# Optimization experiments

Hardware: AMD Instinct MI355X
Metric: run time of the kernel (lower is better)

The kernel has to match this reference:

```python
import jax, jax.numpy as jnp
import numpy as np

NPOINT = 1024
RADIUS = 0.2
NSAMPLE = 32
BN_EPS = 1e-5


def setup_inputs() -> dict:
    key = jax.random.key(0)
    ks = jax.random.split(key, 8)
    B, N, D = 16, 8192, 9
    xyz = jax.random.uniform(ks[0], (B, N, 3), dtype=jnp.float32)
    points = jax.random.normal(ks[1], (B, N, D), dtype=jnp.float32)
    chans = [D, 64, 64, 128]
    inp = {"xyz": xyz, "points": points}
    for i in range(3):
        cin, cout = chans[i], chans[i + 1]
        inp[f"W{i}"] = jax.random.normal(ks[2 + i], (cout, cin), dtype=jnp.float32) / np.sqrt(cin).astype(np.float32)
        inp[f"b{i}"] = jnp.zeros((cout,), jnp.float32)
        inp[f"gamma{i}"] = jnp.ones((cout,), jnp.float32)
        inp[f"beta{i}"] = jnp.zeros((cout,), jnp.float32)
    return inp


def farthest_point_sample(xyz, npoint):
    # xyz: [B,N,3]. Sequential FPS via lax.scan (deterministic start at index 0).
    B, N, _ = xyz.shape
    dist0 = jnp.full((B, N), 1e10, xyz.dtype)
    far0 = jnp.zeros((B,), jnp.int32)

    def step(carry, _):
        distance, farthest = carry
        centroid = jnp.take_along_axis(xyz, farthest[:, None, None], axis=1)  # [B,1,3]
        d = jnp.sum((xyz - centroid) ** 2, axis=-1)  # [B,N]
        distance = jnp.minimum(distance, d)
        return (distance, jnp.argmax(distance, axis=-1).astype(jnp.int32)), farthest

    (_, _), cents = jax.lax.scan(step, (dist0, far0), None, length=npoint)
    return cents.T  # [B,npoint]


def gather_points(points, idx):
    # points [B,N,C], idx [B,...] -> [B,...,C]
    return jax.vmap(lambda p, i: p[i])(points, idx)


def query_ball_point(radius, nsample, xyz, new_xyz):
    # pairwise squared distances [B,S,N]
    sqr = (jnp.sum(new_xyz ** 2, -1)[:, :, None]
           + jnp.sum(xyz ** 2, -1)[:, None, :]
           - 2.0 * jnp.einsum('bsc,bnc->bsn', new_xyz, xyz))
    negd, idx = jax.lax.top_k(-sqr, nsample)  # nsample nearest, ascending distance
    d = -negd
    first = idx[:, :, :1]
    return jnp.where(d > radius ** 2, first, idx)  # [B,S,nsample]


def reference(xyz, points, W0, b0, gamma0, beta0, W1, b1, gamma1, beta1, W2, b2, gamma2, beta2):
    cent = farthest_point_sample(xyz, NPOINT)          # [B,S]
    new_xyz = gather_points(xyz, cent)                  # [B,S,3]
    idx = query_ball_point(RADIUS, NSAMPLE, xyz, new_xyz)
    x = gather_points(points, idx)                      # [B,S,K,D]
    x = jnp.transpose(x, (0, 3, 2, 1))                  # [B,D,K,S]
    for W, b, g, be in ((W0, b0, gamma0, beta0), (W1, b1, gamma1, beta1), (W2, b2, gamma2, beta2)):
        x = jnp.einsum('oc,bcks->boks', W, x) + b[None, :, None, None]
        mean = x.mean(axis=(0, 2, 3), keepdims=True)    # training-mode BatchNorm2d
        var = x.var(axis=(0, 2, 3), keepdims=True)
        x = (x - mean) * jax.lax.rsqrt(var + BN_EPS) * g[None, :, None, None] + be[None, :, None, None]
        x = jax.nn.relu(x)
    feat = jnp.max(x, axis=2)                           # max over nsample -> [B,C,S]
    return new_xyz, jnp.transpose(feat, (0, 2, 1))      # [B,S,3], [B,S,128]
```

## Files before the change

### kernel.cpp

```cpp
#include <hip/hip_runtime.h>
#include <cstddef>
#include <cstdint>


#define BB 16
#define NN 8192
#define DD 9
#define SS 1024
#define KK 32
#define M_COLS (BB*SS*KK)
#define C1 64
#define C2 64
#define C3 128
#define NBKT 64
#define NG 54

#define WSB_IDX   0
#define WSB_STATS (WSB_IDX + M_COLS*2)
#define WSB_AFF   (WSB_STATS + 32768*4)
#define WSB_WT    (WSB_AFF + 512*4)
#define WSB_END   (WSB_WT + 12864*4)
#define WSB_Y2    ((WSB_END + 255) & ~255)
#define PG1 0
#define PS2 (2*NBKT*C1)
#define PQ2 (3*NBKT*C1)
#define PS3 (4*NBKT*C1)
#define PQ3 (PS3 + NBKT*C3)

__device__ __forceinline__ unsigned wave_umax_dpp(unsigned v) {
    int x = (int)v, t;
    t = __builtin_amdgcn_update_dpp(x, x, 0x111, 0xf, 0xf, false);
    x = ((unsigned)t > (unsigned)x) ? t : x;
    t = __builtin_amdgcn_update_dpp(x, x, 0x112, 0xf, 0xf, false);
    x = ((unsigned)t > (unsigned)x) ? t : x;
    t = __builtin_amdgcn_update_dpp(x, x, 0x114, 0xf, 0xf, false);
    x = ((unsigned)t > (unsigned)x) ? t : x;
    t = __builtin_amdgcn_update_dpp(x, x, 0x118, 0xf, 0xf, false);
    x = ((unsigned)t > (unsigned)x) ? t : x;
    t = __builtin_amdgcn_update_dpp(x, x, 0x142, 0xf, 0xf, false);
    x = ((unsigned)t > (unsigned)x) ? t : x;
    t = __builtin_amdgcn_update_dpp(x, x, 0x143, 0xf, 0xf, false);
    x = ((unsigned)t > (unsigned)x) ? t : x;
    return (unsigned)__builtin_amdgcn_readlane(x, 63);
}

#define FPS_T   512
#define FPS_PPT (NN/FPS_T)
#define FPS_W   (FPS_T/64)

__global__ __launch_bounds__(FPS_T) void fps_kernel(const float* __restrict__ xyz,
                                                    float* __restrict__ out_newxyz) {
    __shared__ float sx[NN], sy[NN], sz[NN];
    __shared__ int   sfar[SS];
    __shared__ unsigned long long rp[2][FPS_W];
    const int b = blockIdx.x, tid = threadIdx.x;
    const int wave = tid >> 6, lane = tid & 63;
    const float* base = xyz + (size_t)b * NN * 3;
    for (int i = tid; i < NN; i += FPS_T) {
        sx[i] = base[i*3+0];
        sy[i] = base[i*3+1];
        sz[i] = base[i*3+2];
    }
    __syncthreads();
    float px[FPS_PPT], py[FPS_PPT], pz[FPS_PPT], dist[FPS_PPT];
#pragma unroll
    for (int m = 0; m < FPS_PPT; ++m) {
        int i = tid + m*FPS_T;
        px[m] = sx[i]; py[m] = sy[i]; pz[m] = sz[i];
        dist[m] = 1e10f;
    }
    if (tid == 0) sfar[0] = 0;
    float cx = sx[0], cy = sy[0], cz = sz[0];
    for (int it = 1; it < SS; ++it) {
        float lv = -1.0f; int lm = 0;
#pragma unroll
        for (int m = 0; m < FPS_PPT; ++m) {
            float dx = px[m]-cx, dy = py[m]-cy, dz = pz[m]-cz;
            float d  = fmaf(dz, dz, fmaf(dy, dy, dx*dx));
            float nd = fminf(dist[m], d);
            dist[m] = nd;
            if (nd > lv) { lv = nd; lm = m; }
        }
        int li = tid + lm*FPS_T;
        unsigned uv  = __float_as_uint(lv);
        unsigned wvu = wave_umax_dpp(uv);
        unsigned ci  = (uv == wvu) ? (unsigned)(NN - 1 - li) : 0u;
        unsigned cm  = wave_umax_dpp(ci);
        const int pb = it & 1;
        if (lane == 0) rp[pb][wave] = ((unsigned long long)wvu << 32) | cm;
        __syncthreads();
        unsigned long long bp = rp[pb][0];
#pragma unroll
        for (int w = 1; w < FPS_W; ++w) {
            unsigned long long o = rp[pb][w];
            bp = (o > bp) ? o : bp;
        }
        int bi = NN - 1 - (int)(unsigned int)(bp & 0xFFFFFFFFull);
        if (tid == 0) sfar[it] = bi;
        cx = sx[bi]; cy = sy[bi]; cz = sz[bi];
    }
    __syncthreads();
    for (int s = tid; s < SS; s += FPS_T) {
        int nidx = sfar[s];
        out_newxyz[((size_t)b*SS + s)*3 + 0] = sx[nidx];
        out_newxyz[((size_t)b*SS + s)*3 + 1] = sy[nidx];
        out_newxyz[((size_t)b*SS + s)*3 + 2] = sz[nidx];
    }
}

__device__ __forceinline__ unsigned fmap(float f) {
    unsigned u = __float_as_uint(f);
    return u ^ (unsigned)(((int)u >> 31) | 0x80000000);
}
#define PK_INF 0xFFFFFFFFFFFFFFFFull

__global__ __launch_bounds__(64) void query_kernel(const float* __restrict__ xyz,
                                                   const float* __restrict__ newxyz,
                                                   unsigned short* __restrict__ idx_out) {
    __shared__ unsigned bm[NN/32];
    const int blk  = blockIdx.x;
    const int b    = blk >> 10;
    const int lane = threadIdx.x;
    for (int i = lane; i < NN/32; i += 64) bm[i] = 0;
    const float cx = newxyz[(size_t)blk*3+0];
    const float cy = newxyz[(size_t)blk*3+1];
    const float cz = newxyz[(size_t)blk*3+2];
    const float s2 = fmaf(cz, cz, fmaf(cy, cy, cx*cx));
    const float* xb = xyz + (size_t)b*NN*3;
    float lv = 3.0e38f; int li = 0;
    for (int m = 0; m < NN/64; ++m) {
        int j = lane + m*64;
        float x = xb[(size_t)j*3+0], y = xb[(size_t)j*3+1], z = xb[(size_t)j*3+2];
        float n2  = fmaf(z, z, fmaf(y, y, x*x));
        float dot = fmaf(cz, z, fmaf(cy, y, cx*x));
        float sq  = (s2 + n2) - 2.0f*dot;
        if (sq < lv) { lv = sq; li = j; }
    }
    __syncthreads();
    unsigned long long lpk = ((unsigned long long)fmap(lv) << 32) | (unsigned)li;
    unsigned long long g = lpk;
#pragma unroll
    for (int msk = 1; msk < 64; msk <<= 1) {
        unsigned long long o = __shfl_xor(g, msk, 64);
        g = (o < g) ? o : g;
    }
    const unsigned R2M = fmap(0.04f);
    int first_idx = 0, out_idx = 0;
    for (int k = 0; k < KK; ++k) {
        int wi = (int)(unsigned)(g & 0xFFFFFFFFull);
        unsigned wm = (unsigned)(g >> 32);
        if (k == 0) first_idx = wi;
        int keep = (wm > R2M) ? first_idx : wi;
        if (lane == k) out_idx = keep;
        int owner = wi & 63;
        if (lane == owner) bm[wi >> 5] |= (1u << (wi & 31));
        __syncthreads();
        int j0 = owner + ((2*lane) << 6);
        int j1 = j0 + 64;
        float x0 = xb[(size_t)j0*3+0], y0 = xb[(size_t)j0*3+1], z0 = xb[(size_t)j0*3+2];
        float x1 = xb[(size_t)j1*3+0], y1 = xb[(size_t)j1*3+1], z1 = xb[(size_t)j1*3+2];
        float sq0 = (s2 + fmaf(z0, z0, fmaf(y0, y0, x0*x0))) - 2.0f*fmaf(cz, z0, fmaf(cy, y0, cx*x0));
        float sq1 = (s2 + fmaf(z1, z1, fmaf(y1, y1, x1*x1))) - 2.0f*fmaf(cz, z1, fmaf(cy, y1, cx*x1));
        bool t0 = (bm[j0 >> 5] >> (j0 & 31)) & 1;
        bool t1 = (bm[j1 >> 5] >> (j1 & 31)) & 1;
        unsigned long long p0 = t0 ? PK_INF : (((unsigned long long)fmap(sq0) << 32) | (unsigned)j0);
        unsigned long long p1 = t1 ? PK_INF : (((unsigned long long)fmap(sq1) << 32) | (unsigned)j1);
        unsigned long long r = (p1 < p0) ? p1 : p0;
        unsigned long long c = (lane == owner) ? PK_INF : lpk;
        c = (r < c) ? r : c;
#pragma unroll
        for (int msk = 1; msk < 64; msk <<= 1) {
            unsigned long long ro = __shfl_xor(r, msk, 64);
            unsigned long long co = __shfl_xor(c, msk, 64);
            r = (ro < r) ? ro : r;
            c = (co < c) ? co : c;
        }
        if (lane == owner) lpk = r;
        g = c;
        __syncthreads();
    }
    if (lane < KK) idx_out[(size_t)blk*KK + lane] = (unsigned short)out_idx;
}

__global__ void transpose_w_kernel(const float* __restrict__ W0, const float* __restrict__ W1,
                                   const float* __restrict__ W2, float* __restrict__ w0t,
                                   float* __restrict__ w1t, float* __restrict__ w2t) {
    int t = blockIdx.x*256 + threadIdx.x;
    if (t < DD*C1)  { int c = t / C1, o = t % C1; w0t[t] = W0[o*DD + c]; }
    if (t < C1*C2)  { int c = t / C2, o = t % C2; w1t[t] = W1[o*C1 + c]; }
    if (t < C1*C3)  { int c = t / C3, o = t % C3; w2t[t] = W2[o*C1 + c]; }
}

__global__ __launch_bounds__(256) void gram_kernel(const float* __restrict__ points,
                                                   const unsigned short* __restrict__ idxw,
                                                   float* __restrict__ pg) {
    __shared__ float sg[NG];
    const int tid = threadIdx.x, lane = tid & 63;
    float acc[NG];
#pragma unroll
    for (int t = 0; t < NG; ++t) acc[t] = 0.f;
#pragma unroll
    for (int i = 0; i < 4; ++i) {
        int col = blockIdx.x*1024 + i*256 + tid;
        int n = idxw[col];
        int b = col >> 15;
        const float* p = points + ((size_t)b*NN + n)*DD;
        float x[DD];
#pragma unroll
        for (int c = 0; c < DD; ++c) x[c] = p[c];
#pragma unroll
        for (int c = 0; c < DD; ++c) acc[c] += x[c];
        int t = DD;
#pragma unroll
        for (int c = 0; c < DD; ++c)
#pragma unroll
            for (int d = c; d < DD; ++d) { acc[t] = fmaf(x[c], x[d], acc[t]); ++t; }
    }
#pragma unroll
    for (int t = 0; t < NG; ++t) {
#pragma unroll
        for (int msk = 1; msk < 64; msk <<= 1) acc[t] += __shfl_xor(acc[t], msk, 64);
    }
    if (tid < NG) sg[tid] = 0.f;
    __syncthreads();
    if (lane == 0) {
#pragma unroll
        for (int t = 0; t < NG; ++t) atomicAdd(&sg[t], acc[t]);
    }
    __syncthreads();
    int bkt = blockIdx.x & (NBKT-1);
    if (tid < NG) atomicAdd(&pg[bkt*64 + tid], sg[tid]);
}

__global__ void affine1_kernel(const float* __restrict__ pg,
                               const float* __restrict__ W0, const float* __restrict__ b0,
                               const float* __restrict__ gamma, const float* __restrict__ beta,
                               float* __restrict__ scale, float* __restrict__ shift) {
    __shared__ float sm[NG];
    int tid = threadIdx.x;
    if (tid < NG) {
        float s = 0.f;
        for (int b = 0; b < NBKT; ++b) s += pg[b*64 + tid];
        sm[tid] = s;
    }
    __syncthreads();
    if (tid < C1) {
        float w[DD];
#pragma unroll
        for (int i = 0; i < DD; ++i) w[i] = W0[tid*DD + i];
        float mv = 0.f;
#pragma unroll
        for (int i = 0; i < DD; ++i) mv = fmaf(w[i], sm[i], mv);
        float q = 0.f;
        int t = DD;
#pragma unroll
        for (int c = 0; c < DD; ++c)
#pragma unroll
            for (int d = c; d < DD; ++d) {
                float coef = w[c]*w[d];
                if (c != d) coef = coef + coef;
                q = fmaf(coef, sm[t], q); ++t;
            }
        float b0v = b0[tid];
        const float M = (float)M_COLS;
        float s_sum = mv + M*b0v;
        float s_sq  = q + 2.f*b0v*mv + M*b0v*b0v;
        const float invM = 1.0f / M;
        float mean = s_sum * invM;
        float var  = s_sq * invM - mean*mean;
        float sc   = gamma[tid] / sqrtf(var + 1e-5f);
        scale[tid] = sc;
        shift[tid] = beta[tid] - mean*sc;
    }
}

__device__ __forceinline__ void stats_accumulate64(const float* acc,
                                                   float* __restrict__ g_sum,
                                                   float* __restrict__ g_sq) {
    __shared__ float s_sum[C1];
    __shared__ float s_sq[C1];
    int tid = threadIdx.x, lane = tid & 63;
    if (tid < C1) { s_sum[tid] = 0.f; s_sq[tid] = 0.f; }
    __syncthreads();
#pragma unroll
    for (int o = 0; o < C1; ++o) {
        float v = acc[o];
        float q = v*v;
#pragma unroll
        for (int msk = 1; msk < 64; msk <<= 1) {
            v += __shfl_xor(v, msk, 64);
            q += __shfl_xor(q, msk, 64);
        }
        if (lane == 0) { atomicAdd(&s_sum[o], v); atomicAdd(&s_sq[o], q); }
    }
    __syncthreads();
    if (tid < C1) { atomicAdd(&g_sum[tid], s_sum[tid]); atomicAdd(&g_sq[tid], s_sq[tid]); }
    __syncthreads();
}

__device__ __forceinline__ void gather_conv1(const float* __restrict__ points,
                                             const unsigned short* __restrict__ idxw,
                                             const float* __restrict__ w0t,
                                             const float* __restrict__ b0,
                                             int col, float (&a1)[C1]) {
    int n = idxw[col];
    int b = col >> 15;
    const float* p = points + ((size_t)b*NN + n)*DD;
    float x[DD];
#pragma unroll
    for (int c = 0; c < DD; ++c) x[c] = p[c];
#pragma unroll
    for (int o = 0; o < C1; ++o) a1[o] = b0[o];
#pragma unroll
    for (int c = 0; c < DD; ++c) {
        float xc = x[c];
#pragma unroll
        for (int o = 0; o < C1; ++o) a1[o] = fmaf(w0t[c*C1+o], xc, a1[o]);
    }
}

__device__ __forceinline__ void conv2_from_a1(float (&a1)[C1],
                                              const float* __restrict__ sc1,
                                              const float* __restrict__ sh1,
                                              const float* __restrict__ w1t,
                                              const float* __restrict__ b1,
                                              float (&a2)[C2]) {
#pragma unroll
    for (int c = 0; c < C1; ++c) a1[c] = fmaxf(fmaf(a1[c], sc1[c], sh1[c]), 0.0f);
#pragma unroll
    for (int o = 0; o < C2; ++o) a2[o] = b1[o];
    for (int c = 0; c < C1; ++c) {
        float xc = a1[c];
#pragma unroll
        for (int o = 0; o < C2; ++o) a2[o] = fmaf(w1t[c*C2+o], xc, a2[o]);
    }
}

__global__ void affine_kernel(const float* __restrict__ psum, const float* __restrict__ psq,
                              const float* __restrict__ gamma, const float* __restrict__ beta,
                              float* __restrict__ scale, float* __restrict__ shift, int nch) {
    int i = threadIdx.x;
    if (i < nch) {
        float s = 0.f, q = 0.f;
        for (int b = 0; b < NBKT; ++b) { s += psum[b*nch + i]; q += psq[b*nch + i]; }
        const float invM = 1.0f / (float)M_COLS;
        float mean = s * invM;
        float var  = q * invM - mean*mean;
        float sc   = gamma[i] / sqrtf(var + 1e-5f);
        scale[i] = sc;
        shift[i] = beta[i] - mean*sc;
    }
}

template<bool STORE>
__device__ __forceinline__ void pass2_body(const float* __restrict__ points,
                                           const unsigned short* __restrict__ idxw,
                                           const float* __restrict__ w0t,
                                           const float* __restrict__ b0,
                                           const float* __restrict__ sc1,
                                           const float* __restrict__ sh1,
                                           const float* __restrict__ w1t,
                                           const float* __restrict__ b1,
                                           float* __restrict__ Y2,
                                           float* __restrict__ pstats) {
    int col = blockIdx.x*256 + threadIdx.x;
    int bkt = blockIdx.x & (NBKT-1);
    float a1[C1], a2[C2];
    gather_conv1(points, idxw, w0t, b0, col, a1);
    conv2_from_a1(a1, sc1, sh1, w1t, b1, a2);
    if (STORE) {
#pragma unroll
        for (int o = 0; o < C2; ++o) Y2[(size_t)o*M_COLS + col] = a2[o];
    }
    stats_accumulate64(a2, pstats + PS2 + bkt*C1, pstats + PQ2 + bkt*C1);
}

__global__ __launch_bounds__(256) void pass2_kernel(const float* __restrict__ points,
                                                    const unsigned short* __restrict__ idxw,
                                                    const float* __restrict__ w0t,
                                                    const float* __restrict__ b0,
                                                    const float* __restrict__ sc1,
                                                    const float* __restrict__ sh1,
                                                    const float* __restrict__ w1t,
                                                    const float* __restrict__ b1,
                                                    float* __restrict__ pstats) {
    pass2_body<false>(points, idxw, w0t, b0, sc1, sh1, w1t, b1, nullptr, pstats);
}

__global__ __launch_bounds__(256) void pass2_store_kernel(const float* __restrict__ points,
                                                          const unsigned short* __restrict__ idxw,
                                                          const float* __restrict__ w0t,
                                                          const float* __restrict__ b0,
                                                          const float* __restrict__ sc1,
                                                          const float* __restrict__ sh1,
                                                          const float* __restrict__ w1t,
                                                          const float* __restrict__ b1,
                                                          float* __restrict__ Y2,
                                                          float* __restrict__ pstats) {
    pass2_body<true>(points, idxw, w0t, b0, sc1, sh1, w1t, b1, Y2, pstats);
}

__device__ __forceinline__ void pass34_tail(float (&a2)[C2],
                                            const float* __restrict__ sc2,
                                            const float* __restrict__ sh2,
                                            const float* __restrict__ w2t,
                                            const float* __restrict__ b2,
                                            const float* __restrict__ gamma2,
                                            float* __restrict__ pool_out,
                                            float* __restrict__ pstats) {
#pragma unroll
    for (int c = 0; c < C2; ++c) a2[c] = fmaxf(fmaf(a2[c], sc2[c], sh2[c]), 0.0f);
    int col = blockIdx.x*256 + threadIdx.x;
    int bkt = blockIdx.x & (NBKT-1);
    int lane = threadIdx.x & 63;
    int bs = col >> 5;
#pragma unroll
    for (int h = 0; h < 2; ++h) {
        float acc[C1];
#pragma unroll
        for (int o = 0; o < C1; ++o) acc[o] = b2[h*C1+o];
        for (int c = 0; c < C2; ++c) {
            float xc = a2[c];
#pragma unroll
            for (int o = 0; o < C1; ++o) acc[o] = fmaf(w2t[c*C3 + h*C1 + o], xc, acc[o]);
        }
#pragma unroll
        for (int o = 0; o < C1; ++o) {
            bool pos = gamma2[h*C1+o] >= 0.f;
            float v = pos ? acc[o] : -acc[o];
#pragma unroll
            for (int msk = 1; msk < 32; msk <<= 1) v = fmaxf(v, __shfl_xor(v, msk, 64));
            if ((lane & 31) == 0) pool_out[(size_t)bs*C3 + h*C1 + o] = pos ? v : -v;
        }
        stats_accumulate64(acc, pstats + PS3 + bkt*C3 + h*C1, pstats + PQ3 + bkt*C3 + h*C1);
    }
}

__global__ __launch_bounds__(256) void pass34_kernel(const float* __restrict__ points,
                                                     const unsigned short* __restrict__ idxw,
                                                     const float* __restrict__ w0t,
                                                     const float* __restrict__ b0,
                                                     const float* __restrict__ sc1,
                                                     const float* __restrict__ sh1,
                                                     const float* __restrict__ w1t,
                                                     const float* __restrict__ b1,
                                                     const float* __restrict__ sc2,
                                                     const float* __restrict__ sh2,
                                                     const float* __restrict__ w2t,
                                                     const float* __restrict__ b2,
                                                     const float* __restrict__ gamma2,
                                                     float* __restrict__ pool_out,
                                                     float* __restrict__ pstats) {
    int col = blockIdx.x*256 + threadIdx.x;
    float a1[C1], a2[C2];
    gather_conv1(points, idxw, w0t, b0, col, a1);
    conv2_from_a1(a1, sc1, sh1, w1t, b1, a2);
    pass34_tail(a2, sc2, sh2, w2t, b2, gamma2, pool_out, pstats);
}

__global__ __launch_bounds__(256) void pass34_cached_kernel(const float* __restrict__ Y2,
                                                            const float* __restrict__ sc2,
                                                            const float* __restrict__ sh2,
                                                            const float* __restrict__ w2t,
                                                            const float* __restrict__ b2,
                                                            const float* __restrict__ gamma2,
                                                            float* __restrict__ pool_out,
                                                            float* __restrict__ pstats) {
    int col = blockIdx.x*256 + threadIdx.x;
    float a2[C2];
#pragma unroll
    for (int o = 0; o < C2; ++o) a2[o] = Y2[(size_t)o*M_COLS + col];
    pass34_tail(a2, sc2, sh2, w2t, b2, gamma2, pool_out, pstats);
}

__global__ __launch_bounds__(256) void bn3relu_kernel(float* __restrict__ pool,
                                                      const float* __restrict__ sc3,
                                                      const float* __restrict__ sh3) {
    int e = blockIdx.x*256 + threadIdx.x;
    int ch = e & (C3-1);
    float v = pool[e];
    pool[e] = fmaxf(fmaf(v, sc3[ch], sh3[ch]), 0.0f);
}

extern "C" void kernel_launch(void* const* d_in, const int* in_sizes, int n_in,
                              void* d_out, int out_size, void* d_ws, size_t ws_size,
                              hipStream_t stream) {
    const float* xyz    = (const float*)d_in[0];
    const float* points = (const float*)d_in[1];
    const float* W0     = (const float*)d_in[2];
    const float* b0     = (const float*)d_in[3];
    const float* gamma0 = (const float*)d_in[4];
    const float* beta0  = (const float*)d_in[5];
    const float* W1     = (const float*)d_in[6];
    const float* b1     = (const float*)d_in[7];
    const float* gamma1 = (const float*)d_in[8];
    const float* beta1  = (const float*)d_in[9];
    const float* W2     = (const float*)d_in[10];
    const float* b2     = (const float*)d_in[11];
    const float* gamma2 = (const float*)d_in[12];
    const float* beta2  = (const float*)d_in[13];

    char* wsb = (char*)d_ws;
    unsigned short* idxw = (unsigned short*)(wsb + WSB_IDX);
    float* pstats = (float*)(wsb + WSB_STATS);
    float* aff = (float*)(wsb + WSB_AFF);
    float* sc1 = aff,       *sh1 = aff + 64;
    float* sc2 = aff + 128, *sh2 = aff + 192;
    float* sc3 = aff + 256, *sh3 = aff + 384;
    float* wT  = (float*)(wsb + WSB_WT);
    float* w0t = wT, *w1t = wT + DD*C1, *w2t = wT + DD*C1 + C1*C2;
    float* Y2  = (float*)(wsb + WSB_Y2);
    const bool use_y2 = ws_size >= (size_t)WSB_Y2 + (size_t)C2 * M_COLS * 4;

    float* out_newxyz = (float*)d_out;
    float* out_feat   = (float*)d_out + (size_t)BB*SS*3;

    hipMemsetAsync(pstats, 0, 32768*sizeof(float), stream);
    fps_kernel<<<dim3(BB), dim3(FPS_T), 0, stream>>>(xyz, out_newxyz);
    transpose_w_kernel<<<dim3(32), dim3(256), 0, stream>>>(W0, W1, W2, w0t, w1t, w2t);
    query_kernel<<<dim3(BB*SS), dim3(64), 0, stream>>>(xyz, out_newxyz, idxw);
    gram_kernel<<<dim3(M_COLS/1024), dim3(256), 0, stream>>>(points, idxw, pstats + PG1);
    affine1_kernel<<<dim3(1), dim3(64), 0, stream>>>(pstats + PG1, W0, b0, gamma0, beta0, sc1, sh1);
    if (use_y2) {
        pass2_store_kernel<<<dim3(M_COLS/256), dim3(256), 0, stream>>>(points, idxw, w0t, b0, sc1, sh1, w1t, b1, Y2, pstats);
        affine_kernel<<<dim3(1), dim3(128), 0, stream>>>(pstats + PS2, pstats + PQ2, gamma1, beta1, sc2, sh2, C2);
        pass34_cached_kernel<<<dim3(M_COLS/256), dim3(256), 0, stream>>>(Y2, sc2, sh2, w2t, b2, gamma2, out_feat, pstats);
    } else {
        pass2_kernel<<<dim3(M_COLS/256), dim3(256), 0, stream>>>(points, idxw, w0t, b0, sc1, sh1, w1t, b1, pstats);
        affine_kernel<<<dim3(1), dim3(128), 0, stream>>>(pstats + PS2, pstats + PQ2, gamma1, beta1, sc2, sh2, C2);
        pass34_kernel<<<dim3(M_COLS/256), dim3(256), 0, stream>>>(points, idxw, w0t, b0, sc1, sh1, w1t, b1, sc2, sh2, w2t, b2, gamma2, out_feat, pstats);
    }
    affine_kernel<<<dim3(1), dim3(128), 0, stream>>>(pstats + PS3, pstats + PQ3, gamma2, beta2, sc3, sh3, C3);
    bn3relu_kernel<<<dim3((BB*SS*C3)/256), dim3(256), 0, stream>>>(out_feat, sc3, sh3);
}
```

Measured before the change: 1.683 ms.

## Widen FPS to 1024 threads with DPP cross-wave argmax; scatter BN stats via LDS

The FPS kernel moves from 512 to 1024 threads per block, so each thread holds fewer points, and the final cross-wave argmax becomes a DPP 64-bit max over 16 lanes instead of a serial loop over wave partials. BN statistic accumulation in the pass kernels drops the 64-channel shuffle-xor butterfly reductions. Each lane now does LDS atomic adds into a padded, lane-rotated 64x65 table, which 64 threads then sum column-wise. This trades many shuffles for LDS atomics and about 33KB of extra shared memory per block, which may cut occupancy in the pass kernels.

```diff
diff --git a/kernel.cpp b/kernel.cpp
--- a/kernel.cpp
+++ b/kernel.cpp
@@ -14,6 +14,7 @@
 #define C3 128
 #define NBKT 64
 #define NG 54
+#define SROW 65
 
 #define WSB_IDX   0
 #define WSB_STATS (WSB_IDX + M_COLS*2)
@@ -44,7 +45,17 @@
     return (unsigned)__builtin_amdgcn_readlane(x, 63);
 }
 
-#define FPS_T   512
+#define DPP_U64_MAX_STEP(ctrl)                                                  \
+    {                                                                           \
+        int thi = __builtin_amdgcn_update_dpp(hi, hi, (ctrl), 0xf, 0xf, false); \
+        int tlo = __builtin_amdgcn_update_dpp(lo, lo, (ctrl), 0xf, 0xf, false); \
+        bool c = ((unsigned)thi > (unsigned)hi) ||                              \
+                 ((thi == hi) && ((unsigned)tlo > (unsigned)lo));               \
+        hi = c ? thi : hi;                                                      \
+        lo = c ? tlo : lo;                                                      \
+    }
+
+#define FPS_T   1024
 #define FPS_PPT (NN/FPS_T)
 #define FPS_W   (FPS_T/64)
 
@@ -89,22 +100,27 @@
         const int pb = it & 1;
         if (lane == 0) rp[pb][wave] = ((unsigned long long)wvu << 32) | cm;
         __syncthreads();
-        unsigned long long bp = rp[pb][0];
-#pragma unroll
-        for (int w = 1; w < FPS_W; ++w) {
-            unsigned long long o = rp[pb][w];
-            bp = (o > bp) ? o : bp;
-        }
-        int bi = NN - 1 - (int)(unsigned int)(bp & 0xFFFFFFFFull);
+        unsigned long long p = rp[pb][lane & 15];
+        int hi = (int)(unsigned)(p >> 32);
+        int lo = (int)(unsigned)(p & 0xFFFFFFFFull);
+        DPP_U64_MAX_STEP(0x111)
+        DPP_U64_MAX_STEP(0x112)
+        DPP_U64_MAX_STEP(0x114)
+        DPP_U64_MAX_STEP(0x118)
+        unsigned blo = (unsigned)__builtin_amdgcn_readlane(lo, 15);
+        int bi = NN - 1 - (int)blo;
         if (tid == 0) sfar[it] = bi;
         cx = sx[bi]; cy = sy[bi]; cz = sz[bi];
     }
     __syncthreads();
-    for (int s = tid; s < SS; s += FPS_T) {
-        int nidx = sfar[s];
-        out_newxyz[((size_t)b*SS + s)*3 + 0] = sx[nidx];
-        out_newxyz[((size_t)b*SS + s)*3 + 1] = sy[nidx];
-        out_newxyz[((size_t)b*SS + s)*3 + 2] = sz[nidx];
+    {
+        int s = tid;
+        if (s < SS) {
+            int nidx = sfar[s];
+            out_newxyz[((size_t)b*SS + s)*3 + 0] = sx[nidx];
+            out_newxyz[((size_t)b*SS + s)*3 + 1] = sy[nidx];
+            out_newxyz[((size_t)b*SS + s)*3 + 2] = sz[nidx];
+        }
     }
 }
 
@@ -274,27 +290,28 @@
     }
 }
 
-__device__ __forceinline__ void stats_accumulate64(const float* acc,
-                                                   float* __restrict__ g_sum,
-                                                   float* __restrict__ g_sq) {
-    __shared__ float s_sum[C1];
-    __shared__ float s_sq[C1];
+__device__ __forceinline__ void stats_scatter64(const float* acc,
+                                                float* __restrict__ ssum,
+                                                float* __restrict__ ssq,
+                                                float* __restrict__ g_sum,
+                                                float* __restrict__ g_sq) {
     int tid = threadIdx.x, lane = tid & 63;
-    if (tid < C1) { s_sum[tid] = 0.f; s_sq[tid] = 0.f; }
+    for (int i = tid; i < 64*SROW; i += 256) { ssum[i] = 0.f; ssq[i] = 0.f; }
     __syncthreads();
 #pragma unroll
     for (int o = 0; o < C1; ++o) {
+        int row = (lane + o) & 63;
         float v = acc[o];
-        float q = v*v;
-#pragma unroll
-        for (int msk = 1; msk < 64; msk <<= 1) {
-            v += __shfl_xor(v, msk, 64);
-            q += __shfl_xor(q, msk, 64);
-        }
-        if (lane == 0) { atomicAdd(&s_sum[o], v); atomicAdd(&s_sq[o], q); }
-    }
-    __syncthreads();
-    if (tid < C1) { atomicAdd(&g_sum[tid], s_sum[tid]); atomicAdd(&g_sq[tid], s_sq[tid]); }
+        atomicAdd(&ssum[row*SROW + o], v);
+        atomicAdd(&ssq[row*SROW + o], v*v);
+    }
+    __syncthreads();
+    if (tid < 64) {
+        float s = 0.f, q = 0.f;
+        for (int r = 0; r < 64; ++r) { s += ssum[r*SROW + tid]; q += ssq[r*SROW + tid]; }
+        atomicAdd(&g_sum[tid], s);
+        atomicAdd(&g_sq[tid], q);
+    }
     __syncthreads();
 }
 
@@ -363,6 +380,8 @@
                                            const float* __restrict__ b1,
                                            float* __restrict__ Y2,
                                            float* __restrict__ pstats) {
+    __shared__ float ssum[64*SROW];
+    __shared__ float ssq[64*SROW];
     int col = blockIdx.x*256 + threadIdx.x;
     int bkt = blockIdx.x & (NBKT-1);
     float a1[C1], a2[C2];
@@ -372,7 +391,7 @@
 #pragma unroll
         for (int o = 0; o < C2; ++o) Y2[(size_t)o*M_COLS + col] = a2[o];
     }
-    stats_accumulate64(a2, pstats + PS2 + bkt*C1, pstats + PQ2 + bkt*C1);
+    stats_scatter64(a2, ssum, ssq, pstats + PS2 + bkt*C1, pstats + PQ2 + bkt*C1);
 }
 
 __global__ __launch_bounds__(256) void pass2_kernel(const float* __restrict__ points,
@@ -408,6 +427,8 @@
                                             const float* __restrict__ gamma2,
                                             float* __restrict__ pool_out,
                                             float* __restrict__ pstats) {
+    __shared__ float ssum[64*SROW];
+    __shared__ float ssq[64*SROW];
 #pragma unroll
     for (int c = 0; c < C2; ++c) a2[c] = fmaxf(fmaf(a2[c], sc2[c], sh2[c]), 0.0f);
     int col = blockIdx.x*256 + threadIdx.x;
@@ -432,7 +453,7 @@
             for (int msk = 1; msk < 32; msk <<= 1) v = fmaxf(v, __shfl_xor(v, msk, 64));
             if ((lane & 31) == 0) pool_out[(size_t)bs*C3 + h*C1 + o] = pos ? v : -v;
         }
-        stats_accumulate64(acc, pstats + PS3 + bkt*C3 + h*C1, pstats + PQ3 + bkt*C3 + h*C1);
+        stats_scatter64(acc, ssum, ssq, pstats + PS3 + bkt*C3 + h*C1, pstats + PQ3 + bkt*C3 + h*C1);
     }
 }
 
```

Result: slower. 2.789 ms (+65.7%).
